# Performance work log

Hardware: AMD Instinct MI355X
Metric: run time of the kernel (lower is better)

## Reference

```python
import math
import jax, jax.numpy as jnp
import numpy as np

EXP_SCALING = 10.0
KEY_SCALE_MAX = math.log(2 ** 16 - 1)


def setup_inputs() -> dict:
    key = jax.random.key(0)
    ks = jax.random.split(key, 5)
    B, T, C, nh = 2, 2048, 1024, 16
    x = jax.random.normal(ks[0], (B, T, C), dtype=jnp.float32)
    W_k = jax.random.normal(ks[1], (C, C), dtype=jnp.float32) * 0.02
    W_v = jax.random.normal(ks[2], (C, C), dtype=jnp.float32) * 0.02
    W_c = jax.random.normal(ks[3], (C, C), dtype=jnp.float32) * 0.02
    # parameter inits exactly as in the torch module
    leaky_key_beta = (jnp.linspace(0.5, 5.0, nh).reshape(1, nh, 1, 1) / EXP_SCALING).astype(jnp.float32)
    key_scale = jnp.ones((1, nh, 1, 1), jnp.float32) / EXP_SCALING
    v_coef = jax.random.uniform(ks[4], (1, nh, 1, 1), dtype=jnp.float32)
    val_scale = jnp.full((1, nh, 1, 1), -0.5 / EXP_SCALING, jnp.float32)
    return dict(x=x, W_k=W_k, W_v=W_v, W_c=W_c, leaky_key_beta=leaky_key_beta,
                key_scale=key_scale, v_coef=v_coef, val_scale=val_scale)


def reference(x, W_k, W_v, W_c, leaky_key_beta, key_scale, v_coef, val_scale):
    B, T, C = x.shape
    nh = leaky_key_beta.shape[1]
    hs = C // nh

    # ---- key featurizer ----
    k = (x @ W_k.T).reshape(B, T, nh, hs).transpose(0, 2, 1, 3)  # [B,nh,T,hs]
    t = jnp.arange(T)
    dec = (t[:, None] - t[None, :])                               # i - j
    causal = dec >= 0
    dec_f = jnp.where(causal, dec, 0).astype(x.dtype)
    beta = jnp.abs(leaky_key_beta).reshape(nh, 1, 1) * EXP_SCALING
    coef = jnp.where(causal[None], jnp.exp(-dec_f[None] * beta), 0.0)  # [nh,T,T] tril exp decay
    k = jnp.einsum('hij,bhjd->bhid', coef, k)                    # leaky average (EMA as matmul)
    k = k / (jnp.linalg.norm(k, axis=-1, keepdims=True) + 1e-10)
    k = k * jnp.exp(jnp.minimum(EXP_SCALING * key_scale, KEY_SCALE_MAX))  # scale_pow = 1

    # ---- value featurizer ----
    v = (x @ W_v.T).reshape(B, T, nh, hs).transpose(0, 2, 1, 3)  # [B,nh,T,hs]
    # F.pad(v, (-1, 1)) on time axis: drop t=0, append zero at end -> v_shift[t] = v[t+1]
    v_shift = jnp.concatenate([v[:, :, 1:], jnp.zeros_like(v[:, :, :1])], axis=2)
    v = (1.0 - v_coef) * v_shift + v_coef * v
    v = v / (jnp.linalg.norm(v, axis=-1, keepdims=True) + 1e-10)
    v = v * jnp.exp(EXP_SCALING * val_scale)

    # ---- shifted-causal SDPA with q = k[:, :, 1:], scale = 1 ----
    q = k[:, :, 1:]                                              # [B,nh,T-1,hs]
    att = jnp.einsum('bhqd,bhkd->bhqk', q, k)                    # [B,nh,T-1,T]
    # query index q (position q+1) attends strictly-past keys j <= q (tril diagonal=-1 shifted)
    mask = t[None, :] <= t[: T - 1, None]                        # [T-1, T]
    att = jnp.where(mask[None, None], att, -jnp.inf)
    att = jax.nn.softmax(att, axis=-1)
    y1 = jnp.einsum('bhqk,bhkd->bhqd', att, v)                   # [B,nh,T-1,hs]
    y = jnp.concatenate([jnp.zeros_like(y1[:, :, :1]), y1], axis=2)  # row 0 is zeros
    y = y.transpose(0, 2, 1, 3).reshape(B, T, C)
    return y @ W_c.T
```

## Files before the change

### kernel.cpp

```cpp
#include <hip/hip_runtime.h>
#include <hip/hip_bf16.h>
#include <math.h>

namespace {

constexpr int kB = 2, kT = 2048, kC = 1024, kNH = 16, kHS = 64;
constexpr int kM = kB * kT;
constexpr int kChunk = 32, kNChunk = kT / kChunk;
constexpr float kES = 10.0f;
constexpr float kKSM = 11.090339630053647f;
constexpr float kMSUB = 7.5f;

typedef __attribute__((ext_vector_type(8))) short bf16x8;
typedef __attribute__((ext_vector_type(4))) float f32x4;
typedef __attribute__((ext_vector_type(8))) unsigned short us8;

__device__ __forceinline__ size_t rowoff(int b, int t) {
  return ((size_t)b * kT + t) * kC;
}

__device__ __forceinline__ unsigned short f2bf(float f) {
  unsigned int u = __float_as_uint(f);
  u += 0x7fffu + ((u >> 16) & 1u);
  return (unsigned short)(u >> 16);
}
__device__ __forceinline__ float bf2f(unsigned short h) {
  return __uint_as_float((unsigned int)h << 16);
}

__device__ __forceinline__ f32x4 mfma16(bf16x8 a, bf16x8 b, f32x4 c) {
  return __builtin_amdgcn_mfma_f32_16x16x32_bf16(a, b, c, 0, 0, 0);
}

__device__ __forceinline__ int cvtpk(float a, float b) {
  int r;
  asm("v_cvt_pk_bf16_f32 %0, %1, %2" : "=v"(r) : "v"(a), "v"(b));
  return r;
}

__device__ __forceinline__ void gload16(const unsigned short* g, unsigned short* l) {
  __builtin_amdgcn_global_load_lds(
      (const __attribute__((address_space(1))) unsigned int*)g,
      (__attribute__((address_space(3))) unsigned int*)l, 16, 0, 0);
}

__device__ __forceinline__ bf16x8 ldsfrag(const unsigned short* arr, int row, int cg) {
  return *(const bf16x8*)&arr[row * 64 + ((cg ^ (row & 7)) << 3)];
}

__global__ __launch_bounds__(256)
void split_all(const float* __restrict__ x, unsigned short* __restrict__ Xhi,
               unsigned short* __restrict__ Xlo,
               const float* __restrict__ Wk, unsigned short* __restrict__ Wkh,
               const float* __restrict__ Wv, unsigned short* __restrict__ Wvh,
               const float* __restrict__ Wc, unsigned short* __restrict__ Wch)
{
  const int bid = blockIdx.x;
  if (bid < 4096) {
    int i = bid * 256 + threadIdx.x;
    float4 v = reinterpret_cast<const float4*>(x)[i];
    ushort4 h, l;
    h.x = f2bf(v.x); l.x = f2bf(v.x - bf2f(h.x));
    h.y = f2bf(v.y); l.y = f2bf(v.y - bf2f(h.y));
    h.z = f2bf(v.z); l.z = f2bf(v.z - bf2f(h.z));
    h.w = f2bf(v.w); l.w = f2bf(v.w - bf2f(h.w));
    reinterpret_cast<ushort4*>(Xhi)[i] = h;
    reinterpret_cast<ushort4*>(Xlo)[i] = l;
  } else {
    const float* src = (bid < 5120) ? Wk : (bid < 6144) ? Wv : Wc;
    unsigned short* dst = (bid < 5120) ? Wkh : (bid < 6144) ? Wvh : Wch;
    int i = ((bid - 4096) & 1023) * 256 + threadIdx.x;
    float4 v = reinterpret_cast<const float4*>(src)[i];
    ushort4 h;
    h.x = f2bf(v.x); h.y = f2bf(v.y); h.z = f2bf(v.z); h.w = f2bf(v.w);
    reinterpret_cast<ushort4*>(dst)[i] = h;
  }
}

__global__ __launch_bounds__(256)
void gemm_kv(const unsigned short* __restrict__ Ah, const unsigned short* __restrict__ Al,
             const unsigned short* __restrict__ Wkh, const unsigned short* __restrict__ Wvh,
             float* __restrict__ Ck, float* __restrict__ Cv)
{
  __shared__ __attribute__((aligned(16))) unsigned short sAh[128 * 64];
  __shared__ __attribute__((aligned(16))) unsigned short sAl[128 * 64];
  __shared__ __attribute__((aligned(16))) unsigned short sBh[128 * 64];
  const int bid = blockIdx.x;
  const int wg = (bid & 7) * 64 + (bid >> 3);
  const int bn = wg & 15, bm = wg >> 4;
  const bool kmode = (bn < 8);
  const unsigned short* __restrict__ Bsrc = kmode ? Wkh : Wvh;
  const int n0 = (kmode ? bn : bn - 8) * 128;
  const int m0 = bm * 128;
  const int tid = threadIdx.x;
  const int w = tid >> 6, lane = tid & 63;
  const int lrow = lane & 15, lg = lane >> 4;
  const int wr = w >> 1, wc = w & 1;
  const int srow = w * 8 + (lane >> 3);
  const int gsh = ((lane & 7) ^ (lane >> 3)) << 3;

  f32x4 acc[4][4];
#pragma unroll
  for (int i = 0; i < 4; ++i)
#pragma unroll
    for (int j = 0; j < 4; ++j) acc[i][j] = f32x4{0.f, 0.f, 0.f, 0.f};

  for (int k0 = 0; k0 < kC; k0 += 64) {
#pragma unroll
    for (int p = 0; p < 4; ++p) {
      const int r = p * 32 + srow;
      const int lb = (p * 32 + w * 8) * 64;
      gload16(&Ah[(size_t)(m0 + r) * kC + k0 + gsh], &sAh[lb]);
      gload16(&Bsrc[(size_t)(n0 + r) * kC + k0 + gsh], &sBh[lb]);
      if (kmode) gload16(&Al[(size_t)(m0 + r) * kC + k0 + gsh], &sAl[lb]);
    }
    __syncthreads();
#pragma unroll
    for (int ksl = 0; ksl < 2; ++ksl) {
      bf16x8 av[4], bv[4];
#pragma unroll
      for (int i = 0; i < 4; ++i)
        av[i] = ldsfrag(sAh, wr * 64 + i * 16 + lrow, ksl * 4 + lg);
#pragma unroll
      for (int j = 0; j < 4; ++j)
        bv[j] = ldsfrag(sBh, wc * 64 + j * 16 + lrow, ksl * 4 + lg);
#pragma unroll
      for (int i = 0; i < 4; ++i)
#pragma unroll
        for (int j = 0; j < 4; ++j)
          acc[i][j] = mfma16(av[i], bv[j], acc[i][j]);
      if (kmode) {
        bf16x8 lv[4];
#pragma unroll
        for (int i = 0; i < 4; ++i)
          lv[i] = ldsfrag(sAl, wr * 64 + i * 16 + lrow, ksl * 4 + lg);
#pragma unroll
        for (int i = 0; i < 4; ++i)
#pragma unroll
          for (int j = 0; j < 4; ++j)
            acc[i][j] = mfma16(lv[i], bv[j], acc[i][j]);
      }
    }
    __syncthreads();
  }

  float* __restrict__ C = kmode ? Ck : Cv;
#pragma unroll
  for (int i = 0; i < 4; ++i)
#pragma unroll
    for (int j = 0; j < 4; ++j)
#pragma unroll
      for (int r = 0; r < 4; ++r) {
        int row = m0 + wr * 64 + i * 16 + lg * 4 + r;
        int col = n0 + wc * 64 + j * 16 + lrow;
        C[(size_t)row * kC + col] = acc[i][j][r];
      }
}

__global__ __launch_bounds__(256)
void gemm_out(const unsigned short* __restrict__ Yh, const unsigned short* __restrict__ Wch,
              float* __restrict__ C)
{
  __shared__ __attribute__((aligned(16))) unsigned short sAh[128 * 64];
  __shared__ __attribute__((aligned(16))) unsigned short sBh[64 * 64];
  const int bid = blockIdx.x;
  const int wg = (bid & 7) * 64 + (bid >> 3);
  const int bn = wg & 15, bm = wg >> 4;
  const int n0 = bn * 64, m0 = bm * 128;
  const int tid = threadIdx.x;
  const int w = tid >> 6, lane = tid & 63;
  const int lrow = lane & 15, lg = lane >> 4;
  const int wr = w >> 1, wc = w & 1;
  const int srow = w * 8 + (lane >> 3);
  const int gsh = ((lane & 7) ^ (lane >> 3)) << 3;

  f32x4 acc[4][2];
#pragma unroll
  for (int i = 0; i < 4; ++i)
#pragma unroll
    for (int j = 0; j < 2; ++j) acc[i][j] = f32x4{0.f, 0.f, 0.f, 0.f};

  for (int k0 = 0; k0 < kC; k0 += 64) {
#pragma unroll
    for (int p = 0; p < 4; ++p) {
      const int r = p * 32 + srow;
      const int lb = (p * 32 + w * 8) * 64;
      gload16(&Yh[(size_t)(m0 + r) * kC + k0 + gsh], &sAh[lb]);
      if (p < 2) gload16(&Wch[(size_t)(n0 + r) * kC + k0 + gsh], &sBh[lb]);
    }
    __syncthreads();
#pragma unroll
    for (int ksl = 0; ksl < 2; ++ksl) {
      bf16x8 av[4], bv[2];
#pragma unroll
      for (int i = 0; i < 4; ++i)
        av[i] = ldsfrag(sAh, wr * 64 + i * 16 + lrow, ksl * 4 + lg);
#pragma unroll
      for (int j = 0; j < 2; ++j)
        bv[j] = ldsfrag(sBh, wc * 32 + j * 16 + lrow, ksl * 4 + lg);
#pragma unroll
      for (int i = 0; i < 4; ++i)
#pragma unroll
        for (int j = 0; j < 2; ++j)
          acc[i][j] = mfma16(av[i], bv[j], acc[i][j]);
    }
    __syncthreads();
  }
#pragma unroll
  for (int i = 0; i < 4; ++i)
#pragma unroll
    for (int j = 0; j < 2; ++j)
#pragma unroll
      for (int r = 0; r < 4; ++r) {
        int row = m0 + wr * 64 + i * 16 + lg * 4 + r;
        int col = n0 + wc * 32 + j * 16 + lrow;
        C[(size_t)row * kC + col] = acc[i][j][r];
      }
}

__global__ __launch_bounds__(64)
void decay_fused(const float* __restrict__ kbuf, const float* __restrict__ lkb,
                 const float* __restrict__ ksc, unsigned short* __restrict__ kbf)
{
  const int blk = blockIdx.x;
  const int d = threadIdx.x;
  const int ch = blk % kNChunk;
  const int h = (blk / kNChunk) % kNH;
  const int b = blk / (kNChunk * kNH);
  const float lam = __expf(-fabsf(lkb[h]) * kES);
  const float kscale = __expf(fminf(kES * ksc[h], kKSM));

  float cprev = 0.f;
  if (ch > 0) {
    float s = 0.f;
    size_t idx = rowoff(b, (ch - 1) * kChunk) + h * kHS + d;
    for (int j = 0; j < kChunk; ++j) {
      s = kbuf[idx] + lam * s;
      idx += kC;
    }
    cprev = s;
  }

  float s = 0.f, lpow = 1.f;
  size_t idx = rowoff(b, ch * kChunk) + h * kHS + d;
  size_t ko = ((size_t)(b * kNH + h) * kT + ch * kChunk) * kHS + d;
  for (int j = 0; j < kChunk; ++j) {
    s = kbuf[idx] + lam * s;
    lpow *= lam;
    float v = s + lpow * cprev;
    float sq = v * v;
#pragma unroll
    for (int o = 1; o < 64; o <<= 1) sq += __shfl_xor(sq, o, 64);
    kbf[ko] = f2bf(v / (sqrtf(sq) + 1e-10f) * kscale);
    idx += kC;
    ko += kHS;
  }
}

__global__ __launch_bounds__(256)
void v_blend_norm_t(const float* __restrict__ vraw, unsigned short* __restrict__ vtbf,
                    const float* __restrict__ vcf, const float* __restrict__ vsc)
{
  __shared__ __attribute__((aligned(16))) unsigned short Ts[64][72];
  const int nt = kT / 64;
  const int t0 = (blockIdx.x % nt) * 64;
  const int h = (blockIdx.x / nt) % kNH;
  const int b = blockIdx.x / (nt * kNH);
  const int w = threadIdx.x >> 6, lane = threadIdx.x & 63;
  const float vc = vcf[h];
  const float sc = __expf(kES * vsc[h]);
  size_t idx = rowoff(b, t0 + w * 16) + h * kHS + lane;
  float cur = vraw[idx];
#pragma unroll
  for (int i = 0; i < 16; ++i) {
    int t = t0 + w * 16 + i;
    float nxt = (t + 1 < kT) ? vraw[idx + kC] : 0.f;
    float v = (1.f - vc) * nxt + vc * cur;
    float sq = v * v;
#pragma unroll
    for (int o = 1; o < 64; o <<= 1) sq += __shfl_xor(sq, o, 64);
    Ts[w * 16 + i][lane] = f2bf(v / (sqrtf(sq) + 1e-10f) * sc);
    cur = nxt;
    idx += kC;
  }
  __syncthreads();
  const int d = threadIdx.x >> 2, tc = (threadIdx.x & 3) * 16;
  us8 o0, o1;
#pragma unroll
  for (int i = 0; i < 8; ++i) o0[i] = Ts[tc + i][d];
#pragma unroll
  for (int i = 0; i < 8; ++i) o1[i] = Ts[tc + 8 + i][d];
  size_t vo = ((size_t)(b * kNH + h) * kHS + d) * kT + t0 + tc;
  *(us8*)&vtbf[vo] = o0;
  *(us8*)&vtbf[vo + 8] = o1;
}

__global__ __launch_bounds__(256)
void attn_mfma(const unsigned short* __restrict__ kbf,
               const unsigned short* __restrict__ vtbf,
               unsigned short* __restrict__ Yhi)
{
  constexpr int LD = 72;
  __shared__ __attribute__((aligned(16))) unsigned short Ks[2][64 * LD];
  __shared__ __attribute__((aligned(16))) unsigned short Vs[2][64 * LD];
  const int f = blockIdx.x;
  const int xcd = f & 7;
  const int g = f >> 3;
  const int bh = xcd * 4 + (g & 3);
  const int qt = 31 - (g >> 2);
  const int b = bh >> 4, h = bh & 15;
  const int tid = threadIdx.x;
  const int w = tid >> 6, lane = tid & 63;
  const int lrow = lane & 15, lg = lane >> 4, lk = lg * 8;
  const size_t kbase = (size_t)bh * kT * kHS;
  const size_t vbase = (size_t)bh * kHS * kT;
  const int srow = tid >> 2, scs = (tid & 3) * 16;
  const int sig = (srow & 32) | ((srow & 4) << 2) | ((srow & 24) >> 1) | (srow & 3);
  const int P0 = qt * 64;

  bf16x8 qf0, qf1;
  {
    size_t qoff = kbase + (size_t)(P0 + w * 16 + lrow) * kHS + lk;
    qf0 = *(const bf16x8*)&kbf[qoff];
    qf1 = *(const bf16x8*)&kbf[qoff + 32];
  }

  f32x4 yac[4];
#pragma unroll
  for (int dt = 0; dt < 4; ++dt) yac[dt] = f32x4{0.f, 0.f, 0.f, 0.f};
  float lacc = 0.f;

  us8 nk0, nk1, nv0, nv1;
  {
    size_t gk = kbase + (size_t)srow * kHS + scs;
    nk0 = *(const us8*)&kbf[gk];
    nk1 = *(const us8*)&kbf[gk + 8];
    size_t gv = vbase + (size_t)srow * kT + scs;
    nv0 = *(const us8*)&vtbf[gv];
    nv1 = *(const us8*)&vtbf[gv + 8];
  }
  *(us8*)&Ks[0][sig * LD + scs] = nk0;
  *(us8*)&Ks[0][sig * LD + scs + 8] = nk1;
  *(us8*)&Vs[0][srow * LD + scs] = nv0;
  *(us8*)&Vs[0][srow * LD + scs + 8] = nv1;
  __syncthreads();

  int cur = 0;
  for (int j0 = 0; j0 <= P0; j0 += 64) {
    const bool more = (j0 + 64 <= P0);
    if (more) {
      size_t gk = kbase + (size_t)(j0 + 64 + srow) * kHS + scs;
      nk0 = *(const us8*)&kbf[gk];
      nk1 = *(const us8*)&kbf[gk + 8];
      size_t gv = vbase + (size_t)srow * kT + j0 + 64 + scs;
      nv0 = *(const us8*)&vtbf[gv];
      nv1 = *(const us8*)&vtbf[gv + 8];
    }

    f32x4 s[4];
    __builtin_amdgcn_s_setprio(1);
#pragma unroll
    for (int kt = 0; kt < 4; ++kt) {
      bf16x8 a0 = *(const bf16x8*)&Ks[cur][(kt * 16 + lrow) * LD + lk];
      bf16x8 a1 = *(const bf16x8*)&Ks[cur][(kt * 16 + lrow) * LD + lk + 32];
      f32x4 z = f32x4{0.f, 0.f, 0.f, 0.f};
      z = mfma16(a0, qf0, z);
      z = mfma16(a1, qf1, z);
      s[kt] = z;
    }
    __builtin_amdgcn_s_setprio(0);

    const int qg = P0 + w * 16 + lrow;
    float p[4][4];
    float psum = 0.f;
#pragma unroll
    for (int kt = 0; kt < 4; ++kt)
#pragma unroll
      for (int r = 0; r < 4; ++r) {
        float pv = __expf(s[kt][r] - kMSUB);
        if (j0 == P0) {
          int kg = j0 + (kt >> 1) * 32 + 8 * lg + ((kt & 1) << 2) + r;
          if (kg >= qg) pv = 0.f;
        }
        psum += pv;
        p[kt][r] = pv;
      }
    lacc += psum;

    union { int i[4]; bf16x8 v; } pa0u, pa1u;
    pa0u.i[0] = cvtpk(p[0][0], p[0][1]);
    pa0u.i[1] = cvtpk(p[0][2], p[0][3]);
    pa0u.i[2] = cvtpk(p[1][0], p[1][1]);
    pa0u.i[3] = cvtpk(p[1][2], p[1][3]);
    pa1u.i[0] = cvtpk(p[2][0], p[2][1]);
    pa1u.i[1] = cvtpk(p[2][2], p[2][3]);
    pa1u.i[2] = cvtpk(p[3][0], p[3][1]);
    pa1u.i[3] = cvtpk(p[3][2], p[3][3]);

    __builtin_amdgcn_s_setprio(1);
#pragma unroll
    for (int dt = 0; dt < 4; ++dt) {
      bf16x8 v0 = *(const bf16x8*)&Vs[cur][(dt * 16 + lrow) * LD + lk];
      bf16x8 v1 = *(const bf16x8*)&Vs[cur][(dt * 16 + lrow) * LD + lk + 32];
      yac[dt] = mfma16(pa0u.v, v0, yac[dt]);
      yac[dt] = mfma16(pa1u.v, v1, yac[dt]);
    }
    __builtin_amdgcn_s_setprio(0);

    if (more) {
      *(us8*)&Ks[cur ^ 1][sig * LD + scs] = nk0;
      *(us8*)&Ks[cur ^ 1][sig * LD + scs + 8] = nk1;
      *(us8*)&Vs[cur ^ 1][srow * LD + scs] = nv0;
      *(us8*)&Vs[cur ^ 1][srow * LD + scs + 8] = nv1;
    }
    __syncthreads();
    cur ^= 1;
  }

  lacc += __shfl_xor(lacc, 16, 64);
  lacc += __shfl_xor(lacc, 32, 64);
#pragma unroll
  for (int r = 0; r < 4; ++r) {
    float lq = __shfl(lacc, (lane & 48) | (lg * 4 + r), 64);
    int qg = P0 + w * 16 + lg * 4 + r;
    float inv = (qg >= 1) ? 1.f / lq : 0.f;
    size_t o = ((size_t)b * kT + qg) * kC + h * kHS;
#pragma unroll
    for (int dt = 0; dt < 4; ++dt)
      Yhi[o + dt * 16 + lrow] = f2bf(yac[dt][r] * inv);
  }
}

}

extern "C" void kernel_launch(void* const* d_in, const int* in_sizes, int n_in,
                              void* d_out, int out_size, void* d_ws, size_t ws_size,
                              hipStream_t stream)
{
  const float* x   = (const float*)d_in[0];
  const float* Wk  = (const float*)d_in[1];
  const float* Wv  = (const float*)d_in[2];
  const float* Wc  = (const float*)d_in[3];
  const float* lkb = (const float*)d_in[4];
  const float* ksc = (const float*)d_in[5];
  const float* vcf = (const float*)d_in[6];
  const float* vsc = (const float*)d_in[7];
  float* out = (float*)d_out;

  float* wsf = (float*)d_ws;
  float* vraw  = wsf;
  unsigned short* shA = (unsigned short*)(wsf + 4325376);
  unsigned short* Xhi = shA;
  unsigned short* Xlo = shA + 4194304;
  unsigned short* kbf  = shA;
  unsigned short* vtbf = shA + 4194304;
  unsigned short* Wkh = (unsigned short*)(wsf + 8519680);
  unsigned short* Wvh = Wkh + 1048576;
  unsigned short* Wch = Wvh + 1048576;
  unsigned short* Yhi = (unsigned short*)vraw;
  float* kbuf = out;

  const int nscan = kB * kNH * kNChunk;

  split_all<<<7168, 256, 0, stream>>>(x, Xhi, Xlo, Wk, Wkh, Wv, Wvh, Wc, Wch);

  gemm_kv<<<512, 256, 0, stream>>>(Xhi, Xlo, Wkh, Wvh, kbuf, vraw);

  decay_fused<<<nscan, 64, 0, stream>>>(kbuf, lkb, ksc, kbf);
  v_blend_norm_t<<<kB * kNH * (kT / 64), 256, 0, stream>>>(vraw, vtbf, vcf, vsc);

  attn_mfma<<<1024, 256, 0, stream>>>(kbf, vtbf, Yhi);

  gemm_out<<<512, 256, 0, stream>>>(Yhi, Wch, out);
}
```

Baseline: 133.3 us.

## Load K/V MFMA fragments directly from global into registers, drop LDS staging

The attention kernel stops staging K and V tiles through double-buffered shared memory with block-wide barriers. Each wave now loads its MFMA operand fragments straight from global memory into registers, prefetching the next tile's fragments while the current one is computed. The diagonal tile is handled once up front and the unmasked past tiles run in a separate loop with no mask check. This removes LDS writes and reads plus __syncthreads, but each of the four waves now fetches the same K/V data separately, which raises global/L2 traffic and register pressure.

```diff
diff --git a/kernel.cpp b/kernel.cpp
--- a/kernel.cpp
+++ b/kernel.cpp
@@ -300,77 +300,68 @@
                const unsigned short* __restrict__ vtbf,
                unsigned short* __restrict__ Yhi)
 {
-  constexpr int LD = 72;
-  __shared__ __attribute__((aligned(16))) unsigned short Ks[2][64 * LD];
-  __shared__ __attribute__((aligned(16))) unsigned short Vs[2][64 * LD];
   const int f = blockIdx.x;
   const int xcd = f & 7;
   const int g = f >> 3;
   const int bh = xcd * 4 + (g & 3);
-  const int qt = 31 - (g >> 2);
+  const int qblk = 31 - (g >> 2);
   const int b = bh >> 4, h = bh & 15;
   const int tid = threadIdx.x;
   const int w = tid >> 6, lane = tid & 63;
   const int lrow = lane & 15, lg = lane >> 4, lk = lg * 8;
+  const int qgrp = qblk * 4 + w;
   const size_t kbase = (size_t)bh * kT * kHS;
   const size_t vbase = (size_t)bh * kHS * kT;
-  const int srow = tid >> 2, scs = (tid & 3) * 16;
-  const int sig = (srow & 32) | ((srow & 4) << 2) | ((srow & 24) >> 1) | (srow & 3);
-  const int P0 = qt * 64;
+  const int qg = qgrp * 16 + lrow;
 
   bf16x8 qf0, qf1;
   {
-    size_t qoff = kbase + (size_t)(P0 + w * 16 + lrow) * kHS + lk;
+    size_t qoff = kbase + (size_t)qg * kHS + lk;
     qf0 = *(const bf16x8*)&kbf[qoff];
     qf1 = *(const bf16x8*)&kbf[qoff + 32];
   }
 
+  const int krow = ((lrow & 12) << 1) | (lrow & 3);
+  const unsigned short* kp[4];
+  const unsigned short* vp[4];
+#pragma unroll
+  for (int kt = 0; kt < 4; ++kt)
+    kp[kt] = kbf + kbase +
+             (size_t)((kt >> 1) * 32 + ((kt & 1) << 2) + krow) * kHS + lk;
+#pragma unroll
+  for (int dt = 0; dt < 4; ++dt)
+    vp[dt] = vtbf + vbase + (size_t)(dt * 16 + lrow) * kT + lk;
+
   f32x4 yac[4];
 #pragma unroll
   for (int dt = 0; dt < 4; ++dt) yac[dt] = f32x4{0.f, 0.f, 0.f, 0.f};
   float lacc = 0.f;
 
-  us8 nk0, nk1, nv0, nv1;
+  bf16x8 Kf[4][2], Vf[4][2];
+
   {
-    size_t gk = kbase + (size_t)srow * kHS + scs;
-    nk0 = *(const us8*)&kbf[gk];
-    nk1 = *(const us8*)&kbf[gk + 8];
-    size_t gv = vbase + (size_t)srow * kT + scs;
-    nv0 = *(const us8*)&vtbf[gv];
-    nv1 = *(const us8*)&vtbf[gv + 8];
-  }
-  *(us8*)&Ks[0][sig * LD + scs] = nk0;
-  *(us8*)&Ks[0][sig * LD + scs + 8] = nk1;
-  *(us8*)&Vs[0][srow * LD + scs] = nv0;
-  *(us8*)&Vs[0][srow * LD + scs + 8] = nv1;
-  __syncthreads();
-
-  int cur = 0;
-  for (int j0 = 0; j0 <= P0; j0 += 64) {
-    const bool more = (j0 + 64 <= P0);
-    if (more) {
-      size_t gk = kbase + (size_t)(j0 + 64 + srow) * kHS + scs;
-      nk0 = *(const us8*)&kbf[gk];
-      nk1 = *(const us8*)&kbf[gk + 8];
-      size_t gv = vbase + (size_t)srow * kT + j0 + 64 + scs;
-      nv0 = *(const us8*)&vtbf[gv];
-      nv1 = *(const us8*)&vtbf[gv + 8];
-    }
-
+    const size_t kd = (size_t)(qblk * 64) * kHS;
+    const int vd = qblk * 64;
+#pragma unroll
+    for (int kt = 0; kt < 4; ++kt) {
+      Kf[kt][0] = *(const bf16x8*)(kp[kt] + kd);
+      Kf[kt][1] = *(const bf16x8*)(kp[kt] + kd + 32);
+    }
+#pragma unroll
+    for (int dt = 0; dt < 4; ++dt) {
+      Vf[dt][0] = *(const bf16x8*)(vp[dt] + vd);
+      Vf[dt][1] = *(const bf16x8*)(vp[dt] + vd + 32);
+    }
     f32x4 s[4];
     __builtin_amdgcn_s_setprio(1);
 #pragma unroll
     for (int kt = 0; kt < 4; ++kt) {
-      bf16x8 a0 = *(const bf16x8*)&Ks[cur][(kt * 16 + lrow) * LD + lk];
-      bf16x8 a1 = *(const bf16x8*)&Ks[cur][(kt * 16 + lrow) * LD + lk + 32];
       f32x4 z = f32x4{0.f, 0.f, 0.f, 0.f};
-      z = mfma16(a0, qf0, z);
-      z = mfma16(a1, qf1, z);
+      z = mfma16(Kf[kt][0], qf0, z);
+      z = mfma16(Kf[kt][1], qf1, z);
       s[kt] = z;
     }
     __builtin_amdgcn_s_setprio(0);
-
-    const int qg = P0 + w * 16 + lrow;
     float p[4][4];
     float psum = 0.f;
 #pragma unroll
@@ -378,15 +369,12 @@
 #pragma unroll
       for (int r = 0; r < 4; ++r) {
         float pv = __expf(s[kt][r] - kMSUB);
-        if (j0 == P0) {
-          int kg = j0 + (kt >> 1) * 32 + 8 * lg + ((kt & 1) << 2) + r;
-          if (kg >= qg) pv = 0.f;
-        }
+        int kg = qblk * 64 + (kt >> 1) * 32 + 8 * lg + ((kt & 1) << 2) + r;
+        if (kg >= qg) pv = 0.f;
         psum += pv;
         p[kt][r] = pv;
       }
     lacc += psum;
-
     union { int i[4]; bf16x8 v; } pa0u, pa1u;
     pa0u.i[0] = cvtpk(p[0][0], p[0][1]);
     pa0u.i[1] = cvtpk(p[0][2], p[0][3]);
@@ -396,25 +384,82 @@
     pa1u.i[1] = cvtpk(p[2][2], p[2][3]);
     pa1u.i[2] = cvtpk(p[3][0], p[3][1]);
     pa1u.i[3] = cvtpk(p[3][2], p[3][3]);
-
     __builtin_amdgcn_s_setprio(1);
 #pragma unroll
     for (int dt = 0; dt < 4; ++dt) {
-      bf16x8 v0 = *(const bf16x8*)&Vs[cur][(dt * 16 + lrow) * LD + lk];
-      bf16x8 v1 = *(const bf16x8*)&Vs[cur][(dt * 16 + lrow) * LD + lk + 32];
-      yac[dt] = mfma16(pa0u.v, v0, yac[dt]);
-      yac[dt] = mfma16(pa1u.v, v1, yac[dt]);
+      yac[dt] = mfma16(pa0u.v, Vf[dt][0], yac[dt]);
+      yac[dt] = mfma16(pa1u.v, Vf[dt][1], yac[dt]);
     }
     __builtin_amdgcn_s_setprio(0);
-
-    if (more) {
-      *(us8*)&Ks[cur ^ 1][sig * LD + scs] = nk0;
-      *(us8*)&Ks[cur ^ 1][sig * LD + scs + 8] = nk1;
-      *(us8*)&Vs[cur ^ 1][srow * LD + scs] = nv0;
-      *(us8*)&Vs[cur ^ 1][srow * LD + scs + 8] = nv1;
-    }
-    __syncthreads();
-    cur ^= 1;
+  }
+
+  if (qblk > 0) {
+#pragma unroll
+    for (int kt = 0; kt < 4; ++kt) {
+      Kf[kt][0] = *(const bf16x8*)kp[kt];
+      Kf[kt][1] = *(const bf16x8*)(kp[kt] + 32);
+    }
+#pragma unroll
+    for (int dt = 0; dt < 4; ++dt) {
+      Vf[dt][0] = *(const bf16x8*)vp[dt];
+      Vf[dt][1] = *(const bf16x8*)(vp[dt] + 32);
+    }
+    for (int jt = 0; jt < qblk; ++jt) {
+      const size_t kadv = (jt + 1 < qblk) ? (size_t)(64 * kHS) : 0;
+      const int vadv = (jt + 1 < qblk) ? 64 : 0;
+
+      f32x4 s[4];
+      __builtin_amdgcn_s_setprio(1);
+#pragma unroll
+      for (int kt = 0; kt < 4; ++kt) {
+        f32x4 z = f32x4{0.f, 0.f, 0.f, 0.f};
+        z = mfma16(Kf[kt][0], qf0, z);
+        z = mfma16(Kf[kt][1], qf1, z);
+        s[kt] = z;
+      }
+      __builtin_amdgcn_s_setprio(0);
+#pragma unroll
+      for (int kt = 0; kt < 4; ++kt) {
+        kp[kt] += kadv;
+        Kf[kt][0] = *(const bf16x8*)kp[kt];
+        Kf[kt][1] = *(const bf16x8*)(kp[kt] + 32);
+      }
+
+      float p[4][4];
+      float psum = 0.f;
+#pragma unroll
+      for (int kt = 0; kt < 4; ++kt)
+#pragma unroll
+        for (int r = 0; r < 4; ++r) {
+          float pv = __expf(s[kt][r] - kMSUB);
+          psum += pv;
+          p[kt][r] = pv;
+        }
+      lacc += psum;
+      union { int i[4]; bf16x8 v; } pa0u, pa1u;
+      pa0u.i[0] = cvtpk(p[0][0], p[0][1]);
+      pa0u.i[1] = cvtpk(p[0][2], p[0][3]);
+      pa0u.i[2] = cvtpk(p[1][0], p[1][1]);
+      pa0u.i[3] = cvtpk(p[1][2], p[1][3]);
+      pa1u.i[0] = cvtpk(p[2][0], p[2][1]);
+      pa1u.i[1] = cvtpk(p[2][2], p[2][3]);
+      pa1u.i[2] = cvtpk(p[3][0], p[3][1]);
+      pa1u.i[3] = cvtpk(p[3][2], p[3][3]);
+
+      __builtin_amdgcn_s_setprio(1);
+#pragma unroll
+      for (int dt = 0; dt < 4; ++dt) {
+        yac[dt] = mfma16(pa0u.v, Vf[dt][0], yac[dt]);
+        yac[dt] = mfma16(pa1u.v, Vf[dt][1], yac[dt]);
+      }
+      __builtin_amdgcn_s_setprio(0);
+#pragma unroll
+      for (int dt = 0; dt < 4; ++dt) {
+        vp[dt] += vadv;
+        Vf[dt][0] = *(const bf16x8*)vp[dt];
+        Vf[dt][1] = *(const bf16x8*)(vp[dt] + 32);
+      }
+    }
   }
 
   lacc += __shfl_xor(lacc, 16, 64);
@@ -422,9 +467,9 @@
 #pragma unroll
   for (int r = 0; r < 4; ++r) {
     float lq = __shfl(lacc, (lane & 48) | (lg * 4 + r), 64);
-    int qg = P0 + w * 16 + lg * 4 + r;
-    float inv = (qg >= 1) ? 1.f / lq : 0.f;
-    size_t o = ((size_t)b * kT + qg) * kC + h * kHS;
+    int qr = qgrp * 16 + lg * 4 + r;
+    float inv = (qr >= 1) ? 1.f / lq : 0.f;
+    size_t o = ((size_t)b * kT + qr) * kC + h * kHS;
 #pragma unroll
     for (int dt = 0; dt < 4; ++dt)
       Yhi[o + dt * 16 + lrow] = f2bf(yac[dt][r] * inv);
```

New measurement: 226.9 us. 70.2% more time.
